# Kernel optimization log

Hardware: AMD Instinct MI355X
Metric: run time of the kernel (lower is better)

Reference implementation:

```python
import jax, jax.numpy as jnp
import numpy as np

N = 40000   # num nodes
C = 128     # in_channels
H = 8       # num_heads
D = C // H  # head_dim = 16
E = 640000  # num edges
FF = 4 * C


def layer_norm(x, g, b, eps=1e-5):
    m = jnp.mean(x, axis=-1, keepdims=True)
    v = jnp.mean((x - m) ** 2, axis=-1, keepdims=True)
    return (x - m) / jnp.sqrt(v + eps) * g + b


def setup_inputs() -> dict:
    key = jax.random.key(0)
    ks = jax.random.split(key, 16)
    s = 0.02
    x = jax.random.normal(ks[0], (N, C), dtype=jnp.float32)
    edge_index = jax.random.randint(ks[1], (2, E), 0, N, dtype=jnp.int64)
    return {
        'x': x,
        'edge_index': edge_index,
        'Wq': jax.random.normal(ks[2], (C, C), jnp.float32) * s,
        'bq': jnp.zeros((C,), jnp.float32),
        'Wk': jax.random.normal(ks[3], (C, C), jnp.float32) * s,
        'bk': jnp.zeros((C,), jnp.float32),
        'Wv': jax.random.normal(ks[4], (C, C), jnp.float32) * s,
        'bv': jnp.zeros((C,), jnp.float32),
        'Wo': jax.random.normal(ks[5], (C, C), jnp.float32) * s,
        'bo': jnp.zeros((C,), jnp.float32),
        'ln1_g': jnp.ones((C,), jnp.float32),
        'ln1_b': jnp.zeros((C,), jnp.float32),
        'ln2_g': jnp.ones((C,), jnp.float32),
        'ln2_b': jnp.zeros((C,), jnp.float32),
        'W1': jax.random.normal(ks[6], (C, FF), jnp.float32) * s,
        'b1': jnp.zeros((FF,), jnp.float32),
        'W2': jax.random.normal(ks[7], (FF, C), jnp.float32) * s,
        'b2': jnp.zeros((C,), jnp.float32),
    }


def reference(x, edge_index, Wq, bq, Wk, bk, Wv, bv, Wo, bo,
              ln1_g, ln1_b, ln2_g, ln2_b, W1, b1, W2, b2):
    residual = x
    xn = layer_norm(x, ln1_g, ln1_b)
    q = (xn @ Wq + bq).reshape(N, H, D)
    k = (xn @ Wk + bk).reshape(N, H, D)
    v = (xn @ Wv + bv).reshape(N, H, D)
    src, dst = edge_index[0], edge_index[1]
    # per-edge scores: [E, H]
    scores = jnp.einsum('ehd,ehd->eh', q[dst], k[src]) / jnp.sqrt(jnp.float32(D))
    # NOTE: faithful to the source — softmax over ALL edges (dim=0), not per-destination
    attn = jax.nn.softmax(scores, axis=0)[:, :, None]          # [E, H, 1]
    weighted = v[src] * attn                                   # [E, H, D]
    aggregated = jax.ops.segment_sum(weighted, dst, num_segments=N)  # [N, H, D]
    out = aggregated.reshape(N, C) @ Wo + bo
    x1 = residual + out
    residual2 = x1
    xn2 = layer_norm(x1, ln2_g, ln2_b)
    ffn = jax.nn.relu(xn2 @ W1 + b1) @ W2 + b2
    return residual2 + ffn
```

## Files before the change

kernel.cpp:

```cpp
#include <hip/hip_runtime.h>
#include <math.h>

#define NNODES 40000
#define CCH    128
#define NH     8
#define HD     16
#define NEDGE  640000
#define NBLK   157
#define FBLK   10000
#define RBLK   40
#define EBLK   313

typedef __attribute__((ext_vector_type(8))) short bf16x8;
typedef __attribute__((ext_vector_type(4))) float f32x4;
typedef __attribute__((ext_vector_type(2))) float f32x2;

__device__ inline unsigned short f2bf(float f) {
  union { float f; unsigned u; } c; c.f = f;
  unsigned r = c.u + 0x7fffu + ((c.u >> 16) & 1u);
  return (unsigned short)(r >> 16);
}
__device__ inline float bfs(unsigned short u) { union { unsigned i; float f; } c; c.i = (unsigned)u << 16; return c.f; }
__device__ inline float bflo(unsigned u) { union { unsigned i; float f; } c; c.i = u << 16; return c.f; }
__device__ inline float bfhi(unsigned u) { union { unsigned i; float f; } c; c.i = u & 0xffff0000u; return c.f; }

__device__ inline unsigned char f2fp8(float v) {
#if __has_builtin(__builtin_amdgcn_cvt_pk_fp8_f32)
  return (unsigned char)(__builtin_amdgcn_cvt_pk_fp8_f32(v, v, 0, false) & 0xff);
#else
  union { float f; unsigned u; } c; c.f = v;
  unsigned s = (c.u >> 24) & 0x80;
  int e = (int)((c.u >> 23) & 0xff) - 127;
  unsigned m = c.u & 0x7fffff;
  if (e > 8) return s | 0x7e;
  if (e >= -6) {
    unsigned q = (m + 0x80000) >> 20; unsigned ee = e + 7;
    if (q == 8) { q = 0; ee++; }
    if (ee > 15) return s | 0x7e;
    return s | (ee << 3) | q;
  }
  if (e < -10) return (unsigned char)s;
  float a = fabsf(v); unsigned q = (unsigned)(a * 512.f + 0.5f); if (q > 7) q = 7;
  return s | q;
#endif
}
__device__ inline void fp8x4d(unsigned w, float* o) {
#if __has_builtin(__builtin_amdgcn_cvt_pk_f32_fp8)
  f32x2 lo = __builtin_amdgcn_cvt_pk_f32_fp8((int)w, false);
  f32x2 hi = __builtin_amdgcn_cvt_pk_f32_fp8((int)w, true);
  o[0] = lo[0]; o[1] = lo[1]; o[2] = hi[0]; o[3] = hi[1];
#else
  #pragma unroll
  for (int i = 0; i < 4; i++) {
    unsigned b = (w >> (8 * i)) & 0xff;
    unsigned s = b >> 7, e = (b >> 3) & 15, m = b & 7;
    float v;
    if (e) { union { unsigned u; float f; } c; c.u = ((e + 120) << 23) | (m << 20); v = c.f; }
    else v = m * (1.f / 512.f);
    o[i] = s ? -v : v;
  }
#endif
}

__global__ __launch_bounds__(256) void k_wprep_all(const float* __restrict__ Wq,
                                                   const float* __restrict__ Wk,
                                                   const float* __restrict__ Wv,
                                                   const float* __restrict__ W1,
                                                   const float* __restrict__ W2,
                                                   const float* __restrict__ bq,
                                                   const float* __restrict__ bk,
                                                   const float* __restrict__ bv,
                                                   unsigned short* __restrict__ Wqkvt,
                                                   unsigned short* __restrict__ W1t,
                                                   unsigned short* __restrict__ W2t,
                                                   float* __restrict__ bqkv,
                                                   int* __restrict__ deg) {
  int g0 = blockIdx.x * 256 + threadIdx.x;
  if (g0 < NNODES) deg[g0] = 0;
  int idx = g0;
  if (idx < 16384) { int n = idx >> 7, k = idx & 127; Wqkvt[idx] = f2bf(Wq[(size_t)k * 128 + n]); return; }
  idx -= 16384;
  if (idx < 16384) { int n = idx >> 7, k = idx & 127; Wqkvt[16384 + (n << 7) + k] = f2bf(Wk[(size_t)k * 128 + n]); return; }
  idx -= 16384;
  if (idx < 16384) { int n = idx >> 7, k = idx & 127; Wqkvt[32768 + (n << 7) + k] = f2bf(Wv[(size_t)k * 128 + n]); return; }
  idx -= 16384;
  if (idx < 65536) { int n = idx >> 7, k = idx & 127; W1t[idx] = f2bf(W1[(size_t)k * 512 + n]); return; }
  idx -= 65536;
  if (idx < 65536) { int n = idx >> 9, k = idx & 511; W2t[idx] = f2bf(W2[(size_t)k * 128 + n]); return; }
  idx -= 65536;
  if (idx < 384) bqkv[idx] = idx < 128 ? bq[idx] : (idx < 256 ? bk[idx - 128] : bv[idx - 256]);
}

__global__ __launch_bounds__(256) void k_reduce_part(const float* __restrict__ hpart,
                                                     float* __restrict__ dpart) {
  const int t = threadIdx.x;
  const int h = t & 7;
  const int r0 = blockIdx.x * (FBLK / RBLK);
  float s = 0.f;
  for (int r = r0 + (t >> 3); r < r0 + FBLK / RBLK; r += 32) s += hpart[r * 8 + h];
  #pragma unroll
  for (int d = 8; d < 64; d <<= 1) s += __shfl_xor(s, d);
  __shared__ float ws4[4][8];
  int lane = t & 63, wv = t >> 6;
  if (lane < 8) ws4[wv][lane] = s;
  __syncthreads();
  if (t < 8) dpart[blockIdx.x * 8 + t] = ws4[0][t] + ws4[1][t] + ws4[2][t] + ws4[3][t];
}

__global__ __launch_bounds__(256) void k_wprep_wo(const float* __restrict__ W,
                                                  const float* __restrict__ dpart,
                                                  unsigned short* __restrict__ Wt) {
  __shared__ float sinv[8];
  if (threadIdx.x < 64) {
    int h = threadIdx.x & 7;
    float s = 0.f;
    for (int r = threadIdx.x >> 3; r < RBLK; r += 8) s += dpart[r * 8 + h];
    #pragma unroll
    for (int d = 8; d < 64; d <<= 1) s += __shfl_xor(s, d);
    if (threadIdx.x < 8) sinv[h] = 1.0f / s;
  }
  __syncthreads();
  int idx = blockIdx.x * 256 + threadIdx.x;
  if (idx >= CCH * CCH) return;
  int n = idx >> 7, k = idx & 127;
  Wt[idx] = f2bf(W[(size_t)k * CCH + n] * sinv[k >> 4]);
}

template <int NT, int OUTMODE, bool LNA, bool RELU>
__global__ __launch_bounds__(256) void k_gemm128(const void* __restrict__ Ain,
                                                 const unsigned short* __restrict__ Bt,
                                                 const float* __restrict__ bias,
                                                 const float* __restrict__ lng,
                                                 const float* __restrict__ lnb,
                                                 void* __restrict__ outp) {
  __shared__ unsigned short As[64 * 128];
  __shared__ unsigned short Bs[128 * 128];
  const int tid  = threadIdx.x;
  const int row0 = blockIdx.x * 64;
  const int l    = tid & 63;
  const int w    = tid >> 6;
  const int wr   = w >> 1;
  const int wc   = w & 1;

  if (LNA) {
    const float* x = (const float*)Ain;
    int r = tid >> 2, qt = tid & 3;
    const float4* xr = (const float4*)(x + (size_t)(row0 + r) * 128 + qt * 32);
    float4 xv[8];
    float s = 0.f, ss = 0.f;
    #pragma unroll
    for (int i = 0; i < 8; i++) {
      xv[i] = xr[i];
      s  += xv[i].x + xv[i].y + xv[i].z + xv[i].w;
      ss += xv[i].x * xv[i].x + xv[i].y * xv[i].y + xv[i].z * xv[i].z + xv[i].w * xv[i].w;
    }
    s += __shfl_xor(s, 1); ss += __shfl_xor(ss, 1);
    s += __shfl_xor(s, 2); ss += __shfl_xor(ss, 2);
    float mean = s * (1.f / 128.f);
    float var  = ss * (1.f / 128.f) - mean * mean;
    float rstd = rsqrtf(var + 1e-5f);
    #pragma unroll
    for (int i = 0; i < 8; i += 2) {
      int c0 = qt * 32 + i * 4;
      float va[8] = {xv[i].x, xv[i].y, xv[i].z, xv[i].w,
                     xv[i+1].x, xv[i+1].y, xv[i+1].z, xv[i+1].w};
      unsigned short tmp[8];
      #pragma unroll
      for (int u = 0; u < 8; u++)
        tmp[u] = f2bf((va[u] - mean) * rstd * lng[c0 + u] + lnb[c0 + u]);
      int slot = c0 >> 3;
      *(uint4*)(As + r * 128 + ((slot ^ (r & 7)) * 8)) = *(uint4*)tmp;
    }
  } else {
    const unsigned short* A = (const unsigned short*)Ain;
    #pragma unroll
    for (int it = 0; it < 4; it++) {
      int idx = it * 256 + tid;
      int r = idx >> 4, sl = idx & 15;
      uint4 vv = *(const uint4*)(A + (size_t)(row0 + r) * 128 + sl * 8);
      *(uint4*)(As + r * 128 + ((sl ^ (r & 7)) * 8)) = vv;
    }
  }

  #pragma unroll
  for (int t = 0; t < NT; t++) {
    __syncthreads();
    #pragma unroll
    for (int it = 0; it < 8; it++) {
      int idx = it * 256 + tid;
      int n = idx >> 4, sl = idx & 15;
      uint4 vv = *(const uint4*)(Bt + (size_t)(t * 128 + n) * 128 + sl * 8);
      *(uint4*)(Bs + n * 128 + ((sl ^ (n & 7)) * 8)) = vv;
    }
    __syncthreads();

    f32x4 acc[2][4] = {};
    #pragma unroll
    for (int kk = 0; kk < 4; kk++) {
      int sb = kk * 4 + (l >> 4);
      bf16x8 af[2], bfr[4];
      #pragma unroll
      for (int mi = 0; mi < 2; mi++) {
        int r = wr * 32 + mi * 16 + (l & 15);
        af[mi] = *(const bf16x8*)(As + r * 128 + ((sb ^ (r & 7)) * 8));
      }
      #pragma unroll
      for (int ni = 0; ni < 4; ni++) {
        int n = wc * 64 + ni * 16 + (l & 15);
        bfr[ni] = *(const bf16x8*)(Bs + n * 128 + ((sb ^ (n & 7)) * 8));
      }
      #pragma unroll
      for (int mi = 0; mi < 2; mi++)
        #pragma unroll
        for (int ni = 0; ni < 4; ni++)
          acc[mi][ni] = __builtin_amdgcn_mfma_f32_16x16x32_bf16(af[mi], bfr[ni], acc[mi][ni], 0, 0, 0);
    }

    #pragma unroll
    for (int mi = 0; mi < 2; mi++) {
      #pragma unroll
      for (int p = 0; p < 4; p++) {
        int r = row0 + wr * 32 + mi * 16 + (l >> 4) * 4 + p;
        #pragma unroll
        for (int ni = 0; ni < 4; ni++) {
          int cc = wc * 64 + ni * 16 + (l & 15);
          int c  = t * 128 + cc;
          float val = acc[mi][ni][p] + bias[c];
          if (RELU) val = fmaxf(val, 0.f);
          if (OUTMODE == 1) {
            ((unsigned short*)outp)[(size_t)r * (NT * 128) + c] = f2bf(val);
          } else {
            char* rowb = (char*)outp + (size_t)r * 512;
            if (t == 0)      *(unsigned short*)(rowb + cc * 2) = f2bf(val);
            else if (t == 1) *(unsigned char*)(rowb + 256 + cc) = f2fp8(val);
            else             *(unsigned char*)(rowb + 384 + cc) = f2fp8(val);
          }
        }
      }
    }
  }
}

__global__ __launch_bounds__(256, 1) void k_ffn(const unsigned short* __restrict__ xn2,
                                                const unsigned short* __restrict__ W1t,
                                                const unsigned short* __restrict__ W2t,
                                                const float* __restrict__ b1,
                                                const float* __restrict__ b2,
                                                const unsigned short* __restrict__ x1b,
                                                float* __restrict__ outp) {
  __shared__ unsigned short As[64 * 128];
  __shared__ unsigned short Fs[64 * 512];
  __shared__ unsigned short Bs[128 * 128];
  const int tid  = threadIdx.x;
  const int row0 = blockIdx.x * 64;
  const int l    = tid & 63;
  const int w    = tid >> 6;
  const int wr   = w >> 1;
  const int wc   = w & 1;

  #pragma unroll
  for (int it = 0; it < 4; it++) {
    int idx = it * 256 + tid;
    int r = idx >> 4, sl = idx & 15;
    uint4 vv = *(const uint4*)(xn2 + (size_t)(row0 + r) * 128 + sl * 8);
    *(uint4*)(As + r * 128 + ((sl ^ (r & 7)) * 8)) = vv;
  }

  #pragma unroll
  for (int t = 0; t < 4; t++) {
    __syncthreads();
    #pragma unroll
    for (int it = 0; it < 8; it++) {
      int idx = it * 256 + tid;
      int n = idx >> 4, sl = idx & 15;
      uint4 vv = *(const uint4*)(W1t + (size_t)(t * 128 + n) * 128 + sl * 8);
      *(uint4*)(Bs + n * 128 + ((sl ^ (n & 7)) * 8)) = vv;
    }
    __syncthreads();

    f32x4 acc[2][4] = {};
    #pragma unroll
    for (int kk = 0; kk < 4; kk++) {
      int sb = kk * 4 + (l >> 4);
      bf16x8 af[2], bfr[4];
      #pragma unroll
      for (int mi = 0; mi < 2; mi++) {
        int r = wr * 32 + mi * 16 + (l & 15);
        af[mi] = *(const bf16x8*)(As + r * 128 + ((sb ^ (r & 7)) * 8));
      }
      #pragma unroll
      for (int ni = 0; ni < 4; ni++) {
        int n = wc * 64 + ni * 16 + (l & 15);
        bfr[ni] = *(const bf16x8*)(Bs + n * 128 + ((sb ^ (n & 7)) * 8));
      }
      #pragma unroll
      for (int mi = 0; mi < 2; mi++)
        #pragma unroll
        for (int ni = 0; ni < 4; ni++)
          acc[mi][ni] = __builtin_amdgcn_mfma_f32_16x16x32_bf16(af[mi], bfr[ni], acc[mi][ni], 0, 0, 0);
    }

    #pragma unroll
    for (int mi = 0; mi < 2; mi++) {
      #pragma unroll
      for (int p = 0; p < 4; p++) {
        int r = wr * 32 + mi * 16 + (l >> 4) * 4 + p;
        #pragma unroll
        for (int ni = 0; ni < 4; ni++) {
          int cc = wc * 64 + ni * 16 + (l & 15);
          int c  = t * 128 + cc;
          float val = fmaxf(acc[mi][ni][p] + b1[c], 0.f);
          int gs = c >> 3;
          Fs[r * 512 + ((gs ^ (r & 7)) * 8) + (c & 7)] = f2bf(val);
        }
      }
    }
  }

  f32x4 acc2[2][4] = {};
  #pragma unroll
  for (int kc = 0; kc < 8; kc++) {
    __syncthreads();
    #pragma unroll
    for (int it = 0; it < 4; it++) {
      int idx = it * 256 + tid;
      int n = idx >> 3, sl = idx & 7;
      uint4 vv = *(const uint4*)(W2t + (size_t)n * 512 + kc * 64 + sl * 8);
      *(uint4*)(Bs + n * 64 + ((sl ^ (n & 7)) * 8)) = vv;
    }
    __syncthreads();
    #pragma unroll
    for (int kk = 0; kk < 2; kk++) {
      int sb = kk * 4 + (l >> 4);
      bf16x8 af[2], bfr[4];
      #pragma unroll
      for (int mi = 0; mi < 2; mi++) {
        int r = wr * 32 + mi * 16 + (l & 15);
        int gs = kc * 8 + sb;
        af[mi] = *(const bf16x8*)(Fs + r * 512 + ((gs ^ (r & 7)) * 8));
      }
      #pragma unroll
      for (int ni = 0; ni < 4; ni++) {
        int n = wc * 64 + ni * 16 + (l & 15);
        bfr[ni] = *(const bf16x8*)(Bs + n * 64 + ((sb ^ (n & 7)) * 8));
      }
      #pragma unroll
      for (int mi = 0; mi < 2; mi++)
        #pragma unroll
        for (int ni = 0; ni < 4; ni++)
          acc2[mi][ni] = __builtin_amdgcn_mfma_f32_16x16x32_bf16(af[mi], bfr[ni], acc2[mi][ni], 0, 0, 0);
    }
  }

  #pragma unroll
  for (int mi = 0; mi < 2; mi++) {
    #pragma unroll
    for (int p = 0; p < 4; p++) {
      int r = row0 + wr * 32 + mi * 16 + (l >> 4) * 4 + p;
      #pragma unroll
      for (int ni = 0; ni < 4; ni++) {
        int c = wc * 64 + ni * 16 + (l & 15);
        float val = acc2[mi][ni][p] + b2[c] + bfs(x1b[(size_t)r * 128 + c]);
        outp[(size_t)r * 128 + c] = val;
      }
    }
  }
}

template <bool RELU, int RESMODE, int MODE>
__global__ __launch_bounds__(256) void k_mgemm(const unsigned short* __restrict__ A,
                                               const unsigned short* __restrict__ Bt,
                                               const float* __restrict__ bias,
                                               const void* __restrict__ res,
                                               void* __restrict__ outp,
                                               int K, int Nc,
                                               const float* __restrict__ lng,
                                               const float* __restrict__ lnb,
                                               void* __restrict__ outp2) {
  __shared__ unsigned short As[64 * 64];
  __shared__ unsigned short Bs[128 * 64];
  const int tid  = threadIdx.x;
  const int row0 = blockIdx.x * 64;
  const int c0   = blockIdx.y * 128;
  const int l    = tid & 63;
  const int w    = tid >> 6;
  const int wr   = w >> 1;
  const int wc   = w & 1;

  f32x4 acc[2][4] = {};

  for (int kc = 0; kc < K; kc += 64) {
    __syncthreads();
    #pragma unroll
    for (int it = 0; it < 2; it++) {
      int idx = it * 256 + tid;
      int r = idx >> 3, s = idx & 7;
      uint4 vv = *(const uint4*)(A + (size_t)(row0 + r) * K + kc + s * 8);
      *(uint4*)(As + r * 64 + ((s ^ (r & 7)) * 8)) = vv;
    }
    #pragma unroll
    for (int it = 0; it < 4; it++) {
      int idx = it * 256 + tid;
      int n = idx >> 3, s = idx & 7;
      uint4 vv = *(const uint4*)(Bt + (size_t)(c0 + n) * K + kc + s * 8);
      *(uint4*)(Bs + n * 64 + ((s ^ (n & 7)) * 8)) = vv;
    }
    __syncthreads();
    #pragma unroll
    for (int kk = 0; kk < 2; kk++) {
      int sb = kk * 4 + (l >> 4);
      bf16x8 af[2], bfr[4];
      #pragma unroll
      for (int mi = 0; mi < 2; mi++) {
        int r = wr * 32 + mi * 16 + (l & 15);
        af[mi] = *(const bf16x8*)(As + r * 64 + ((sb ^ (r & 7)) * 8));
      }
      #pragma unroll
      for (int ni = 0; ni < 4; ni++) {
        int n = wc * 64 + ni * 16 + (l & 15);
        bfr[ni] = *(const bf16x8*)(Bs + n * 64 + ((sb ^ (n & 7)) * 8));
      }
      #pragma unroll
      for (int mi = 0; mi < 2; mi++)
        #pragma unroll
        for (int ni = 0; ni < 4; ni++)
          acc[mi][ni] = __builtin_amdgcn_mfma_f32_16x16x32_bf16(af[mi], bfr[ni], acc[mi][ni], 0, 0, 0);
    }
  }

  if constexpr (MODE == 3) {
    __shared__ float lnS[64][2], lnSS[64][2], gS[128], bS[128];
    if (tid < 128) { gS[tid] = lng[tid]; bS[tid] = lnb[tid]; }
    #pragma unroll
    for (int mi = 0; mi < 2; mi++) {
      #pragma unroll
      for (int p = 0; p < 4; p++) {
        int lr = wr * 32 + mi * 16 + (l >> 4) * 4 + p;
        int r  = row0 + lr;
        float s = 0.f, ss = 0.f;
        #pragma unroll
        for (int ni = 0; ni < 4; ni++) {
          int c = wc * 64 + ni * 16 + (l & 15);
          float val = acc[mi][ni][p] + bias[c] + ((const float*)res)[(size_t)r * 128 + c];
          acc[mi][ni][p] = val;
          s += val; ss += val * val;
        }
        #pragma unroll
        for (int d = 1; d < 16; d <<= 1) { s += __shfl_xor(s, d); ss += __shfl_xor(ss, d); }
        if ((l & 15) == 0) { lnS[lr][wc] = s; lnSS[lr][wc] = ss; }
      }
    }
    __syncthreads();
    #pragma unroll
    for (int mi = 0; mi < 2; mi++) {
      #pragma unroll
      for (int p = 0; p < 4; p++) {
        int lr = wr * 32 + mi * 16 + (l >> 4) * 4 + p;
        int r  = row0 + lr;
        float m   = (lnS[lr][0] + lnS[lr][1]) * (1.f / 128.f);
        float var = (lnSS[lr][0] + lnSS[lr][1]) * (1.f / 128.f) - m * m;
        float rstd = rsqrtf(var + 1e-5f);
        #pragma unroll
        for (int ni = 0; ni < 4; ni++) {
          int c = wc * 64 + ni * 16 + (l & 15);
          float val = acc[mi][ni][p];
          ((unsigned short*)outp)[(size_t)r * 128 + c]  = f2bf(val);
          ((unsigned short*)outp2)[(size_t)r * 128 + c] = f2bf((val - m) * rstd * gS[c] + bS[c]);
        }
      }
    }
  } else {
    #pragma unroll
    for (int mi = 0; mi < 2; mi++) {
      #pragma unroll
      for (int p = 0; p < 4; p++) {
        int r = row0 + wr * 32 + mi * 16 + (l >> 4) * 4 + p;
        #pragma unroll
        for (int ni = 0; ni < 4; ni++) {
          int c = c0 + wc * 64 + ni * 16 + (l & 15);
          float val = acc[mi][ni][p] + bias[c];
          if (RESMODE == 1) val += ((const float*)res)[(size_t)r * Nc + c];
          if (RESMODE == 2) val += bfs(((const unsigned short*)res)[(size_t)r * Nc + c]);
          if (RELU) val = fmaxf(val, 0.f);
          ((float*)outp)[(size_t)r * Nc + c] = val;
        }
      }
    }
  }
}

__global__ __launch_bounds__(256) void k_histrank(const int* __restrict__ ei,
                                                  int* __restrict__ deg,
                                                  int* __restrict__ rank) {
  int base = blockIdx.x * 2048 + threadIdx.x;
  #pragma unroll
  for (int u = 0; u < 8; u++) {
    int e = base + u * 256;
    if (e < NEDGE) rank[e] = atomicAdd(&deg[ei[NEDGE + e]], 1);
  }
}

__global__ __launch_bounds__(256) void k_scan3a(const int* __restrict__ deg,
                                                int* __restrict__ bsum) {
  int i = blockIdx.x * 256 + threadIdx.x;
  int d = (i < NNODES) ? deg[i] : 0;
  #pragma unroll
  for (int s = 1; s < 64; s <<= 1) d += __shfl_xor(d, s);
  __shared__ int ws4[4];
  if ((threadIdx.x & 63) == 0) ws4[threadIdx.x >> 6] = d;
  __syncthreads();
  if (threadIdx.x == 0) bsum[blockIdx.x] = ws4[0] + ws4[1] + ws4[2] + ws4[3];
}

__global__ __launch_bounds__(256) void k_scan3c(const int* __restrict__ deg,
                                                const int* __restrict__ bsum,
                                                int* __restrict__ off) {
  const int t = threadIdx.x;
  __shared__ int ws4[4];
  __shared__ int sbase;
  {
    int lim = blockIdx.x < NBLK ? blockIdx.x : NBLK;
    int v = (t < lim) ? bsum[t] : 0;
    #pragma unroll
    for (int s = 1; s < 64; s <<= 1) v += __shfl_xor(v, s);
    if ((t & 63) == 0) ws4[t >> 6] = v;
    __syncthreads();
    if (t == 0) sbase = ws4[0] + ws4[1] + ws4[2] + ws4[3];
    __syncthreads();
  }
  int i = blockIdx.x * 256 + t;
  int d = (i < NNODES) ? deg[i] : 0;
  int lane = t & 63, wv = t >> 6;
  int incl = d;
  #pragma unroll
  for (int s = 1; s < 64; s <<= 1) { int o = __shfl_up(incl, s); if (lane >= s) incl += o; }
  __syncthreads();
  if (lane == 63) ws4[wv] = incl;
  __syncthreads();
  int base = sbase;
  for (int w2 = 0; w2 < wv; w2++) base += ws4[w2];
  int ex = base + incl - d;
  if (i < NNODES) off[i] = ex;
  if (i == 0) off[NNODES] = NEDGE;
}

__global__ __launch_bounds__(256) void k_scatter(const int* __restrict__ ei,
                                                 const int* __restrict__ off,
                                                 const int* __restrict__ rank,
                                                 int* __restrict__ srcs) {
  int base = blockIdx.x * 2048 + threadIdx.x;
  #pragma unroll
  for (int u = 0; u < 8; u++) {
    int e = base + u * 256;
    if (e < NEDGE) srcs[off[ei[NEDGE + e]] + rank[e]] = ei[e];
  }
}

__global__ __launch_bounds__(256) void k_fused(const unsigned char* __restrict__ qkv,
                                               const int* __restrict__ off,
                                               const int* __restrict__ srcs,
                                               unsigned* __restrict__ U,
                                               float* __restrict__ hpart) {
  const int wave = threadIdx.x >> 6;
  const int lane = threadIdx.x & 63;
  const int n  = blockIdx.x * 4 + wave;
  const int g  = lane >> 3;
  const int c8 = lane & 7;

  const uint4* qp = (const uint4*)(qkv + (size_t)n * 512 + c8 * 32);
  uint4 qa = qp[0], qb = qp[1];
  float qf[16];
  qf[0]=bflo(qa.x);  qf[1]=bfhi(qa.x);  qf[2]=bflo(qa.y);  qf[3]=bfhi(qa.y);
  qf[4]=bflo(qa.z);  qf[5]=bfhi(qa.z);  qf[6]=bflo(qa.w);  qf[7]=bfhi(qa.w);
  qf[8]=bflo(qb.x);  qf[9]=bfhi(qb.x);  qf[10]=bflo(qb.y); qf[11]=bfhi(qb.y);
  qf[12]=bflo(qb.z); qf[13]=bfhi(qb.z); qf[14]=bflo(qb.w); qf[15]=bfhi(qb.w);

  float acc[16];
  #pragma unroll
  for (int i = 0; i < 16; i++) acc[i] = 0.f;
  float lsum = 0.f;

  const int i0 = off[n], i1 = off[n + 1];
  if (i1 > i0) {
    int j0 = i0 + g; if (j0 >= i1) j0 = i1 - 1;
    int sA = srcs[j0];
    int sB;
    {
      int j1 = i0 + 8 + g;
      if (j1 >= i1) j1 = i1 - 1;
      sB = srcs[j1];
    }
    const uint4* kpA = (const uint4*)(qkv + (size_t)sA * 512 + 256 + c8 * 16);
    uint4 kw = kpA[0], vw = kpA[8];

    for (int jb = i0; jb < i1; jb += 8) {
      uint4 kc = kw, vc = vw;
      bool valid = jb + g < i1;
      if (jb + 8 < i1) {
        const uint4* kpB = (const uint4*)(qkv + (size_t)sB * 512 + 256 + c8 * 16);
        kw = kpB[0]; vw = kpB[8];
      }
      if (jb + 16 < i1) {
        int j2 = jb + 16 + g;
        if (j2 >= i1) j2 = i1 - 1;
        sB = srcs[j2];
      }
      float kf[16], vf[16];
      fp8x4d(kc.x, kf + 0); fp8x4d(kc.y, kf + 4); fp8x4d(kc.z, kf + 8); fp8x4d(kc.w, kf + 12);
      fp8x4d(vc.x, vf + 0); fp8x4d(vc.y, vf + 4); fp8x4d(vc.z, vf + 8); fp8x4d(vc.w, vf + 12);
      float p = 0.f;
      #pragma unroll
      for (int i = 0; i < 16; i++) p += qf[i] * kf[i];
      float w = valid ? __expf(p * 0.25f) : 0.f;
      lsum += w;
      #pragma unroll
      for (int i = 0; i < 16; i++) acc[i] += w * vf[i];
    }
  }

  #pragma unroll
  for (int d = 8; d < 64; d <<= 1) {
    #pragma unroll
    for (int i = 0; i < 16; i++) acc[i] += __shfl_xor(acc[i], d);
    lsum += __shfl_xor(lsum, d);
  }

  __shared__ float wsum[4][8];
  if (lane < 8) {
    wsum[wave][c8] = lsum;
    unsigned o[8];
    #pragma unroll
    for (int i = 0; i < 8; i++)
      o[i] = ((unsigned)f2bf(acc[2 * i + 1]) << 16) | f2bf(acc[2 * i]);
    uint4* up = (uint4*)(U + (size_t)n * 64 + c8 * 8);
    up[0] = make_uint4(o[0], o[1], o[2], o[3]);
    up[1] = make_uint4(o[4], o[5], o[6], o[7]);
  }
  __syncthreads();
  if (threadIdx.x < 8) {
    hpart[blockIdx.x * 8 + threadIdx.x] =
        wsum[0][threadIdx.x] + wsum[1][threadIdx.x] + wsum[2][threadIdx.x] + wsum[3][threadIdx.x];
  }
}

extern "C" void kernel_launch(void* const* d_in, const int* in_sizes, int n_in,
                              void* d_out, int out_size, void* d_ws, size_t ws_size,
                              hipStream_t stream) {
  const float* x    = (const float*)d_in[0];
  const int*   ei   = (const int*)d_in[1];
  const float* Wq   = (const float*)d_in[2];
  const float* bq   = (const float*)d_in[3];
  const float* Wk   = (const float*)d_in[4];
  const float* bk   = (const float*)d_in[5];
  const float* Wv   = (const float*)d_in[6];
  const float* bv   = (const float*)d_in[7];
  const float* Wo   = (const float*)d_in[8];
  const float* bo   = (const float*)d_in[9];
  const float* ln1g = (const float*)d_in[10];
  const float* ln1b = (const float*)d_in[11];
  const float* ln2g = (const float*)d_in[12];
  const float* ln2b = (const float*)d_in[13];
  const float* W1   = (const float*)d_in[14];
  const float* b1   = (const float*)d_in[15];
  const float* W2   = (const float*)d_in[16];
  const float* b2   = (const float*)d_in[17];
  float* out = (float*)d_out;

  char* p = (char*)d_ws;
  const size_t NCb = (size_t)NNODES * CCH * 2;
  unsigned short* xn2  = (unsigned short*)p; p += NCb;
  unsigned char*  qkvb = (unsigned char*)p;  p += (size_t)NNODES * 512;
  unsigned short* agg  = (unsigned short*)p; p += NCb;
  unsigned short* x1b  = (unsigned short*)p; p += NCb;
  int* deg    = (int*)p;                     p += (size_t)NNODES * 4 + 256;
  int* off    = (int*)p;                     p += (size_t)(NNODES + 1) * 4 + 256;
  int* rank   = (int*)p;                     p += (size_t)NEDGE * 4;
  int* srcs   = (int*)p;                     p += (size_t)NEDGE * 4;
  int* bsum   = (int*)p;                     p += 256 * 4;
  float* hpart = (float*)p;                  p += (size_t)FBLK * 8 * 4;
  float* dpart = (float*)p;                  p += (size_t)RBLK * 8 * 4 + 256;
  float* bqkv  = (float*)p;                  p += 384 * 4 + 256;
  unsigned short* Wqkvt = (unsigned short*)p; p += (size_t)384 * CCH * 2;
  unsigned short* Wot   = (unsigned short*)p; p += (size_t)CCH * CCH * 2;
  unsigned short* W1t   = (unsigned short*)p; p += (size_t)CCH * 4 * CCH * 2;
  unsigned short* W2t   = (unsigned short*)p; p += (size_t)CCH * 4 * CCH * 2;

  dim3 blk(256);
  dim3 gM(NNODES / 64, 1);

  k_wprep_all<<<706, blk, 0, stream>>>(Wq, Wk, Wv, W1, W2, bq, bk, bv,
                                       Wqkvt, W1t, W2t, bqkv, deg);

  k_histrank<<<EBLK, blk, 0, stream>>>(ei, deg, rank);
  k_scan3a<<<NBLK, blk, 0, stream>>>(deg, bsum);
  k_scan3c<<<NBLK, blk, 0, stream>>>(deg, bsum, off);
  k_scatter<<<EBLK, blk, 0, stream>>>(ei, off, rank, srcs);

  k_gemm128<3, 2, true, false><<<gM, blk, 0, stream>>>(x, Wqkvt, bqkv,
                                                       ln1g, ln1b, qkvb);

  k_fused<<<FBLK, blk, 0, stream>>>(qkvb, off, srcs, (unsigned*)agg, hpart);
  k_reduce_part<<<RBLK, blk, 0, stream>>>(hpart, dpart);

  k_wprep_wo<<<64, blk, 0, stream>>>(Wo, dpart, Wot);
  k_mgemm<false, 1, 3><<<gM, blk, 0, stream>>>(agg, Wot, bo, x, x1b,
                                               CCH, CCH, ln2g, ln2b, xn2);

  k_ffn<<<gM, blk, 0, stream>>>(xn2, W1t, W2t, b1, b2, x1b, out);
}
```

Before: 167.8 us.

## Fuse Wo GEMM, LN2 and FFN1; split FFN2 into separate GEMM

Moves the Wo transpose into the shared weight-prep kernel and applies the softmax normalisation on the fly to the aggregated activations. The Wo projection, residual, second layer norm and first FFN GEMM now run in one kernel that writes the ReLU hidden layer to global memory, and a separate GEMM computes the second FFN layer. This drops one launch and the xn2 round trip, and lowers shared memory per block to allow more occupancy. In exchange it adds a 40000x512 bf16 intermediate write and read. The edge histogram and scatter kernels also get twice as many blocks with half the work each.

```diff
diff --git a/kernel.cpp b/kernel.cpp
--- a/kernel.cpp
+++ b/kernel.cpp
@@ -9,7 +9,7 @@
 #define NBLK   157
 #define FBLK   10000
 #define RBLK   40
-#define EBLK   313
+#define EBLK   625
 
 typedef __attribute__((ext_vector_type(8))) short bf16x8;
 typedef __attribute__((ext_vector_type(4))) float f32x4;
@@ -67,12 +67,14 @@
                                                    const float* __restrict__ Wv,
                                                    const float* __restrict__ W1,
                                                    const float* __restrict__ W2,
+                                                   const float* __restrict__ Wo,
                                                    const float* __restrict__ bq,
                                                    const float* __restrict__ bk,
                                                    const float* __restrict__ bv,
                                                    unsigned short* __restrict__ Wqkvt,
                                                    unsigned short* __restrict__ W1t,
                                                    unsigned short* __restrict__ W2t,
+                                                   unsigned short* __restrict__ Wot,
                                                    float* __restrict__ bqkv,
                                                    int* __restrict__ deg) {
   int g0 = blockIdx.x * 256 + threadIdx.x;
@@ -88,6 +90,8 @@
   idx -= 65536;
   if (idx < 65536) { int n = idx >> 9, k = idx & 511; W2t[idx] = f2bf(W2[(size_t)k * 128 + n]); return; }
   idx -= 65536;
+  if (idx < 16384) { int n = idx >> 7, k = idx & 127; Wot[(n << 7) + k] = f2bf(Wo[(size_t)k * 128 + n]); return; }
+  idx -= 16384;
   if (idx < 384) bqkv[idx] = idx < 128 ? bq[idx] : (idx < 256 ? bk[idx - 128] : bv[idx - 256]);
 }
 
@@ -105,25 +109,6 @@
   if (lane < 8) ws4[wv][lane] = s;
   __syncthreads();
   if (t < 8) dpart[blockIdx.x * 8 + t] = ws4[0][t] + ws4[1][t] + ws4[2][t] + ws4[3][t];
-}
-
-__global__ __launch_bounds__(256) void k_wprep_wo(const float* __restrict__ W,
-                                                  const float* __restrict__ dpart,
-                                                  unsigned short* __restrict__ Wt) {
-  __shared__ float sinv[8];
-  if (threadIdx.x < 64) {
-    int h = threadIdx.x & 7;
-    float s = 0.f;
-    for (int r = threadIdx.x >> 3; r < RBLK; r += 8) s += dpart[r * 8 + h];
-    #pragma unroll
-    for (int d = 8; d < 64; d <<= 1) s += __shfl_xor(s, d);
-    if (threadIdx.x < 8) sinv[h] = 1.0f / s;
-  }
-  __syncthreads();
-  int idx = blockIdx.x * 256 + threadIdx.x;
-  if (idx >= CCH * CCH) return;
-  int n = idx >> 7, k = idx & 127;
-  Wt[idx] = f2bf(W[(size_t)k * CCH + n] * sinv[k >> 4]);
 }
 
 template <int NT, int OUTMODE, bool LNA, bool RELU>
@@ -241,16 +226,24 @@
   }
 }
 
-__global__ __launch_bounds__(256, 1) void k_ffn(const unsigned short* __restrict__ xn2,
-                                                const unsigned short* __restrict__ W1t,
-                                                const unsigned short* __restrict__ W2t,
-                                                const float* __restrict__ b1,
-                                                const float* __restrict__ b2,
-                                                const unsigned short* __restrict__ x1b,
-                                                float* __restrict__ outp) {
-  __shared__ unsigned short As[64 * 128];
-  __shared__ unsigned short Fs[64 * 512];
-  __shared__ unsigned short Bs[128 * 128];
+__global__ __launch_bounds__(256) void k_woln2ffn1(const unsigned short* __restrict__ agg,
+                                                   const unsigned short* __restrict__ Wot,
+                                                   const float* __restrict__ dpart,
+                                                   const float* __restrict__ bo,
+                                                   const float* __restrict__ x,
+                                                   const float* __restrict__ lng,
+                                                   const float* __restrict__ lnb,
+                                                   const unsigned short* __restrict__ W1t,
+                                                   const float* __restrict__ b1,
+                                                   unsigned short* __restrict__ x1b,
+                                                   unsigned short* __restrict__ ffn1) {
+  __shared__ char arena[49152];
+  unsigned short* As   = (unsigned short*)arena;
+  unsigned short* Bs   = (unsigned short*)(arena + 8192);
+  unsigned short* Fs   = (unsigned short*)arena;
+  unsigned short* BsW1 = (unsigned short*)(arena + 16384);
+  __shared__ float lnS[64][2], lnSS[64][2], gS[128], bS[128], sinv[8];
+
   const int tid  = threadIdx.x;
   const int row0 = blockIdx.x * 64;
   const int l    = tid & 63;
@@ -258,12 +251,103 @@
   const int wr   = w >> 1;
   const int wc   = w & 1;
 
-  #pragma unroll
-  for (int it = 0; it < 4; it++) {
-    int idx = it * 256 + tid;
-    int r = idx >> 4, sl = idx & 15;
-    uint4 vv = *(const uint4*)(xn2 + (size_t)(row0 + r) * 128 + sl * 8);
-    *(uint4*)(As + r * 128 + ((sl ^ (r & 7)) * 8)) = vv;
+  {
+    int h = tid & 7;
+    float s = 0.f;
+    for (int r = tid >> 3; r < RBLK; r += 32) s += dpart[r * 8 + h];
+    #pragma unroll
+    for (int d = 8; d < 64; d <<= 1) s += __shfl_xor(s, d);
+    if (tid < 128) { gS[tid] = lng[tid]; bS[tid] = lnb[tid]; }
+    __shared__ float ws4[4][8];
+    int lane = tid & 63, wv = tid >> 6;
+    if (lane < 8) ws4[wv][lane] = s;
+    __syncthreads();
+    if (tid < 8) sinv[tid] = 1.0f / (ws4[0][tid] + ws4[1][tid] + ws4[2][tid] + ws4[3][tid]);
+  }
+
+  f32x4 acc[2][4] = {};
+  for (int kc = 0; kc < 128; kc += 64) {
+    __syncthreads();
+    #pragma unroll
+    for (int it = 0; it < 2; it++) {
+      int idx = it * 256 + tid;
+      int r = idx >> 3, s5 = idx & 7;
+      uint4 vv = *(const uint4*)(agg + (size_t)(row0 + r) * 128 + kc + s5 * 8);
+      float sc = sinv[(kc >> 4) + (s5 >> 1)];
+      unsigned short tmp[8];
+      const unsigned short* pv = (const unsigned short*)&vv;
+      #pragma unroll
+      for (int u = 0; u < 8; u++) tmp[u] = f2bf(bfs(pv[u]) * sc);
+      *(uint4*)(As + r * 64 + ((s5 ^ (r & 7)) * 8)) = *(uint4*)tmp;
+    }
+    #pragma unroll
+    for (int it = 0; it < 4; it++) {
+      int idx = it * 256 + tid;
+      int n = idx >> 3, s5 = idx & 7;
+      uint4 vv = *(const uint4*)(Wot + (size_t)n * 128 + kc + s5 * 8);
+      *(uint4*)(Bs + n * 64 + ((s5 ^ (n & 7)) * 8)) = vv;
+    }
+    __syncthreads();
+    #pragma unroll
+    for (int kk = 0; kk < 2; kk++) {
+      int sb = kk * 4 + (l >> 4);
+      bf16x8 af[2], bfr[4];
+      #pragma unroll
+      for (int mi = 0; mi < 2; mi++) {
+        int r = wr * 32 + mi * 16 + (l & 15);
+        af[mi] = *(const bf16x8*)(As + r * 64 + ((sb ^ (r & 7)) * 8));
+      }
+      #pragma unroll
+      for (int ni = 0; ni < 4; ni++) {
+        int n = wc * 64 + ni * 16 + (l & 15);
+        bfr[ni] = *(const bf16x8*)(Bs + n * 64 + ((sb ^ (n & 7)) * 8));
+      }
+      #pragma unroll
+      for (int mi = 0; mi < 2; mi++)
+        #pragma unroll
+        for (int ni = 0; ni < 4; ni++)
+          acc[mi][ni] = __builtin_amdgcn_mfma_f32_16x16x32_bf16(af[mi], bfr[ni], acc[mi][ni], 0, 0, 0);
+    }
+  }
+
+  #pragma unroll
+  for (int mi = 0; mi < 2; mi++) {
+    #pragma unroll
+    for (int p = 0; p < 4; p++) {
+      int lr = wr * 32 + mi * 16 + (l >> 4) * 4 + p;
+      int r  = row0 + lr;
+      float s = 0.f, ss = 0.f;
+      #pragma unroll
+      for (int ni = 0; ni < 4; ni++) {
+        int c = wc * 64 + ni * 16 + (l & 15);
+        float val = acc[mi][ni][p] + bo[c] + x[(size_t)r * 128 + c];
+        acc[mi][ni][p] = val;
+        s += val; ss += val * val;
+      }
+      #pragma unroll
+      for (int d = 1; d < 16; d <<= 1) { s += __shfl_xor(s, d); ss += __shfl_xor(ss, d); }
+      if ((l & 15) == 0) { lnS[lr][wc] = s; lnSS[lr][wc] = ss; }
+    }
+  }
+  __syncthreads();
+  #pragma unroll
+  for (int mi = 0; mi < 2; mi++) {
+    #pragma unroll
+    for (int p = 0; p < 4; p++) {
+      int lr = wr * 32 + mi * 16 + (l >> 4) * 4 + p;
+      int r  = row0 + lr;
+      float m   = (lnS[lr][0] + lnS[lr][1]) * (1.f / 128.f);
+      float var = (lnSS[lr][0] + lnSS[lr][1]) * (1.f / 128.f) - m * m;
+      float rstd = rsqrtf(var + 1e-5f);
+      #pragma unroll
+      for (int ni = 0; ni < 4; ni++) {
+        int c = wc * 64 + ni * 16 + (l & 15);
+        float val = acc[mi][ni][p];
+        x1b[(size_t)r * 128 + c] = f2bf(val);
+        unsigned short xb = f2bf((val - m) * rstd * gS[c] + bS[c]);
+        Fs[lr * 128 + (((c >> 3) ^ (lr & 7)) * 8) + (c & 7)] = xb;
+      }
+    }
   }
 
   #pragma unroll
@@ -274,11 +358,11 @@
       int idx = it * 256 + tid;
       int n = idx >> 4, sl = idx & 15;
       uint4 vv = *(const uint4*)(W1t + (size_t)(t * 128 + n) * 128 + sl * 8);
-      *(uint4*)(Bs + n * 128 + ((sl ^ (n & 7)) * 8)) = vv;
-    }
-    __syncthreads();
-
-    f32x4 acc[2][4] = {};
+      *(uint4*)(BsW1 + n * 128 + ((sl ^ (n & 7)) * 8)) = vv;
+    }
+    __syncthreads();
+
+    f32x4 acc2[2][4] = {};
     #pragma unroll
     for (int kk = 0; kk < 4; kk++) {
       int sb = kk * 4 + (l >> 4);
@@ -286,97 +370,44 @@
       #pragma unroll
       for (int mi = 0; mi < 2; mi++) {
         int r = wr * 32 + mi * 16 + (l & 15);
-        af[mi] = *(const bf16x8*)(As + r * 128 + ((sb ^ (r & 7)) * 8));
+        af[mi] = *(const bf16x8*)(Fs + r * 128 + ((sb ^ (r & 7)) * 8));
       }
       #pragma unroll
       for (int ni = 0; ni < 4; ni++) {
         int n = wc * 64 + ni * 16 + (l & 15);
-        bfr[ni] = *(const bf16x8*)(Bs + n * 128 + ((sb ^ (n & 7)) * 8));
+        bfr[ni] = *(const bf16x8*)(BsW1 + n * 128 + ((sb ^ (n & 7)) * 8));
       }
       #pragma unroll
       for (int mi = 0; mi < 2; mi++)
         #pragma unroll
         for (int ni = 0; ni < 4; ni++)
-          acc[mi][ni] = __builtin_amdgcn_mfma_f32_16x16x32_bf16(af[mi], bfr[ni], acc[mi][ni], 0, 0, 0);
+          acc2[mi][ni] = __builtin_amdgcn_mfma_f32_16x16x32_bf16(af[mi], bfr[ni], acc2[mi][ni], 0, 0, 0);
     }
 
     #pragma unroll
     for (int mi = 0; mi < 2; mi++) {
       #pragma unroll
       for (int p = 0; p < 4; p++) {
-        int r = wr * 32 + mi * 16 + (l >> 4) * 4 + p;
+        int r = row0 + wr * 32 + mi * 16 + (l >> 4) * 4 + p;
         #pragma unroll
         for (int ni = 0; ni < 4; ni++) {
           int cc = wc * 64 + ni * 16 + (l & 15);
           int c  = t * 128 + cc;
-          float val = fmaxf(acc[mi][ni][p] + b1[c], 0.f);
-          int gs = c >> 3;
-          Fs[r * 512 + ((gs ^ (r & 7)) * 8) + (c & 7)] = f2bf(val);
+          float val = fmaxf(acc2[mi][ni][p] + b1[c], 0.f);
+          ffn1[(size_t)r * 512 + c] = f2bf(val);
         }
       }
     }
   }
-
-  f32x4 acc2[2][4] = {};
-  #pragma unroll
-  for (int kc = 0; kc < 8; kc++) {
-    __syncthreads();
-    #pragma unroll
-    for (int it = 0; it < 4; it++) {
-      int idx = it * 256 + tid;
-      int n = idx >> 3, sl = idx & 7;
-      uint4 vv = *(const uint4*)(W2t + (size_t)n * 512 + kc * 64 + sl * 8);
-      *(uint4*)(Bs + n * 64 + ((sl ^ (n & 7)) * 8)) = vv;
-    }
-    __syncthreads();
-    #pragma unroll
-    for (int kk = 0; kk < 2; kk++) {
-      int sb = kk * 4 + (l >> 4);
-      bf16x8 af[2], bfr[4];
-      #pragma unroll
-      for (int mi = 0; mi < 2; mi++) {
-        int r = wr * 32 + mi * 16 + (l & 15);
-        int gs = kc * 8 + sb;
-        af[mi] = *(const bf16x8*)(Fs + r * 512 + ((gs ^ (r & 7)) * 8));
-      }
-      #pragma unroll
-      for (int ni = 0; ni < 4; ni++) {
-        int n = wc * 64 + ni * 16 + (l & 15);
-        bfr[ni] = *(const bf16x8*)(Bs + n * 64 + ((sb ^ (n & 7)) * 8));
-      }
-      #pragma unroll
-      for (int mi = 0; mi < 2; mi++)
-        #pragma unroll
-        for (int ni = 0; ni < 4; ni++)
-          acc2[mi][ni] = __builtin_amdgcn_mfma_f32_16x16x32_bf16(af[mi], bfr[ni], acc2[mi][ni], 0, 0, 0);
-    }
-  }
-
-  #pragma unroll
-  for (int mi = 0; mi < 2; mi++) {
-    #pragma unroll
-    for (int p = 0; p < 4; p++) {
-      int r = row0 + wr * 32 + mi * 16 + (l >> 4) * 4 + p;
-      #pragma unroll
-      for (int ni = 0; ni < 4; ni++) {
-        int c = wc * 64 + ni * 16 + (l & 15);
-        float val = acc2[mi][ni][p] + b2[c] + bfs(x1b[(size_t)r * 128 + c]);
-        outp[(size_t)r * 128 + c] = val;
-      }
-    }
-  }
-}
-
-template <bool RELU, int RESMODE, int MODE>
+}
+
+template <bool RELU, int RESMODE>
 __global__ __launch_bounds__(256) void k_mgemm(const unsigned short* __restrict__ A,
                                                const unsigned short* __restrict__ Bt,
                                                const float* __restrict__ bias,
                                                const void* __restrict__ res,
-                                               void* __restrict__ outp,
-                                               int K, int Nc,
-                                               const float* __restrict__ lng,
-                                               const float* __restrict__ lnb,
-                                               void* __restrict__ outp2) {
+                                               float* __restrict__ outp,
+                                               int K, int Nc) {
   __shared__ unsigned short As[64 * 64];
   __shared__ unsigned short Bs[128 * 64];
   const int tid  = threadIdx.x;
@@ -428,62 +459,19 @@
     }
   }
 
-  if constexpr (MODE == 3) {
-    __shared__ float lnS[64][2], lnSS[64][2], gS[128], bS[128];
-    if (tid < 128) { gS[tid] = lng[tid]; bS[tid] = lnb[tid]; }
-    #pragma unroll
-    for (int mi = 0; mi < 2; mi++) {
-      #pragma unroll
-      for (int p = 0; p < 4; p++) {
-        int lr = wr * 32 + mi * 16 + (l >> 4) * 4 + p;
-        int r  = row0 + lr;
-        float s = 0.f, ss = 0.f;
-        #pragma unroll
-        for (int ni = 0; ni < 4; ni++) {
-          int c = wc * 64 + ni * 16 + (l & 15);
-          float val = acc[mi][ni][p] + bias[c] + ((const float*)res)[(size_t)r * 128 + c];
-          acc[mi][ni][p] = val;
-          s += val; ss += val * val;
-        }
-        #pragma unroll
-        for (int d = 1; d < 16; d <<= 1) { s += __shfl_xor(s, d); ss += __shfl_xor(ss, d); }
-        if ((l & 15) == 0) { lnS[lr][wc] = s; lnSS[lr][wc] = ss; }
-      }
-    }
-    __syncthreads();
-    #pragma unroll
-    for (int mi = 0; mi < 2; mi++) {
-      #pragma unroll
-      for (int p = 0; p < 4; p++) {
-        int lr = wr * 32 + mi * 16 + (l >> 4) * 4 + p;
-        int r  = row0 + lr;
-        float m   = (lnS[lr][0] + lnS[lr][1]) * (1.f / 128.f);
-        float var = (lnSS[lr][0] + lnSS[lr][1]) * (1.f / 128.f) - m * m;
-        float rstd = rsqrtf(var + 1e-5f);
-        #pragma unroll
-        for (int ni = 0; ni < 4; ni++) {
-          int c = wc * 64 + ni * 16 + (l & 15);
-          float val = acc[mi][ni][p];
-          ((unsigned short*)outp)[(size_t)r * 128 + c]  = f2bf(val);
-          ((unsigned short*)outp2)[(size_t)r * 128 + c] = f2bf((val - m) * rstd * gS[c] + bS[c]);
-        }
-      }
-    }
-  } else {
-    #pragma unroll
-    for (int mi = 0; mi < 2; mi++) {
-      #pragma unroll
-      for (int p = 0; p < 4; p++) {
-        int r = row0 + wr * 32 + mi * 16 + (l >> 4) * 4 + p;
-        #pragma unroll
-        for (int ni = 0; ni < 4; ni++) {
-          int c = c0 + wc * 64 + ni * 16 + (l & 15);
-          float val = acc[mi][ni][p] + bias[c];
-          if (RESMODE == 1) val += ((const float*)res)[(size_t)r * Nc + c];
-          if (RESMODE == 2) val += bfs(((const unsigned short*)res)[(size_t)r * Nc + c]);
-          if (RELU) val = fmaxf(val, 0.f);
-          ((float*)outp)[(size_t)r * Nc + c] = val;
-        }
+  #pragma unroll
+  for (int mi = 0; mi < 2; mi++) {
+    #pragma unroll
+    for (int p = 0; p < 4; p++) {
+      int r = row0 + wr * 32 + mi * 16 + (l >> 4) * 4 + p;
+      #pragma unroll
+      for (int ni = 0; ni < 4; ni++) {
+        int c = c0 + wc * 64 + ni * 16 + (l & 15);
+        float val = acc[mi][ni][p] + bias[c];
+        if (RESMODE == 1) val += ((const float*)res)[(size_t)r * Nc + c];
+        if (RESMODE == 2) val += bfs(((const unsigned short*)res)[(size_t)r * Nc + c]);
+        if (RELU) val = fmaxf(val, 0.f);
+        outp[(size_t)r * Nc + c] = val;
       }
     }
   }
@@ -492,9 +480,9 @@
 __global__ __launch_bounds__(256) void k_histrank(const int* __restrict__ ei,
                                                   int* __restrict__ deg,
                                                   int* __restrict__ rank) {
-  int base = blockIdx.x * 2048 + threadIdx.x;
-  #pragma unroll
-  for (int u = 0; u < 8; u++) {
+  int base = blockIdx.x * 1024 + threadIdx.x;
+  #pragma unroll
+  for (int u = 0; u < 4; u++) {
     int e = base + u * 256;
     if (e < NEDGE) rank[e] = atomicAdd(&deg[ei[NEDGE + e]], 1);
   }
@@ -548,9 +536,9 @@
                                                  const int* __restrict__ off,
                                                  const int* __restrict__ rank,
                                                  int* __restrict__ srcs) {
-  int base = blockIdx.x * 2048 + threadIdx.x;
-  #pragma unroll
-  for (int u = 0; u < 8; u++) {
+  int base = blockIdx.x * 1024 + threadIdx.x;
+  #pragma unroll
+  for (int u = 0; u < 4; u++) {
     int e = base + u * 256;
     if (e < NEDGE) srcs[off[ei[NEDGE + e]] + rank[e]] = ei[e];
   }
@@ -668,10 +656,10 @@
 
   char* p = (char*)d_ws;
   const size_t NCb = (size_t)NNODES * CCH * 2;
-  unsigned short* xn2  = (unsigned short*)p; p += NCb;
   unsigned char*  qkvb = (unsigned char*)p;  p += (size_t)NNODES * 512;
   unsigned short* agg  = (unsigned short*)p; p += NCb;
   unsigned short* x1b  = (unsigned short*)p; p += NCb;
+  unsigned short* ffn1 = (unsigned short*)p; p += (size_t)NNODES * 512 * 2;
   int* deg    = (int*)p;                     p += (size_t)NNODES * 4 + 256;
   int* off    = (int*)p;                     p += (size_t)(NNODES + 1) * 4 + 256;
   int* rank   = (int*)p;                     p += (size_t)NEDGE * 4;
@@ -688,8 +676,8 @@
   dim3 blk(256);
   dim3 gM(NNODES / 64, 1);
 
-  k_wprep_all<<<706, blk, 0, stream>>>(Wq, Wk, Wv, W1, W2, bq, bk, bv,
-                                       Wqkvt, W1t, W2t, bqkv, deg);
+  k_wprep_all<<<770, blk, 0, stream>>>(Wq, Wk, Wv, W1, W2, Wo, bq, bk, bv,
+                                       Wqkvt, W1t, W2t, Wot, bqkv, deg);
 
   k_histrank<<<EBLK, blk, 0, stream>>>(ei, deg, rank);
   k_scan3a<<<NBLK, blk, 0, stream>>>(deg, bsum);
@@ -702,9 +690,9 @@
   k_fused<<<FBLK, blk, 0, stream>>>(qkvb, off, srcs, (unsigned*)agg, hpart);
   k_reduce_part<<<RBLK, blk, 0, stream>>>(hpart, dpart);
 
-  k_wprep_wo<<<64, blk, 0, stream>>>(Wo, dpart, Wot);
-  k_mgemm<false, 1, 3><<<gM, blk, 0, stream>>>(agg, Wot, bo, x, x1b,
-                                               CCH, CCH, ln2g, ln2b, xn2);
-
-  k_ffn<<<gM, blk, 0, stream>>>(xn2, W1t, W2t, b1, b2, x1b, out);
-}
+  k_woln2ffn1<<<gM, blk, 0, stream>>>(agg, Wot, dpart, bo, x, ln2g, ln2b,
+                                      W1t, b1, x1b, ffn1);
+
+  k_mgemm<false, 2><<<gM, blk, 0, stream>>>(ffn1, W2t, b2, x1b, out,
+                                            4 * CCH, CCH);
+}
```

Measured after the change: 155.8 us. 7.1% less time.
